# Optimization experiments

Hardware: AMD Instinct MI355X
Metric: run time of the kernel (lower is better)

The kernel has to match this reference:

```python
import jax, jax.numpy as jnp
import numpy as np

D_MODEL = 2048
NUM_HEADS = 16
HEAD_DIM = D_MODEL // NUM_HEADS
SCALE = 1.0 / np.sqrt(HEAD_DIM).astype(np.float32)
NEG_INF = -1e9


def setup_inputs() -> dict:
    key = jax.random.key(0)
    ks = jax.random.split(key, 10)
    B, S = 2, 2048
    x = jax.random.normal(ks[0], (B, S, D_MODEL), dtype=jnp.float32)
    # causal lower-triangular mask, broadcastable over (B, H)
    causal_mask = jnp.tril(jnp.ones((S, S), dtype=jnp.int32))[None, None]
    init = 1.0 / np.sqrt(D_MODEL)
    def lin(kw, kb):
        W = jax.random.uniform(kw, (D_MODEL, D_MODEL), jnp.float32, -init, init)
        b = jax.random.uniform(kb, (D_MODEL,), jnp.float32, -init, init)
        return W, b
    Wq, bq = lin(ks[1], ks[2])
    Wk, bk = lin(ks[3], ks[4])
    Wv, bv = lin(ks[5], ks[6])
    Wo, bo = lin(ks[7], ks[8])
    return {"x": x, "causal_mask": causal_mask,
            "Wq": Wq, "bq": bq, "Wk": Wk, "bk": bk,
            "Wv": Wv, "bv": bv, "Wo": Wo, "bo": bo}


def reference(x, causal_mask, Wq, bq, Wk, bk, Wv, bv, Wo, bo):
    B, S, _ = x.shape
    def proj(W, b):
        # torch Linear: x @ W.T + b -> (B, H, S, Dh)
        y = jnp.einsum('bsd,ed->bse', x, W) + b
        return y.reshape(B, S, NUM_HEADS, HEAD_DIM).transpose(0, 2, 1, 3)
    q = proj(Wq, bq)
    k = proj(Wk, bk)
    v = proj(Wv, bv)
    # apply_rope is a no-op stub in the source; q, k unchanged.
    scores = jnp.einsum('bhqd,bhkd->bhqk', q, k) * SCALE
    scores = jnp.where(causal_mask == 0, NEG_INF, scores)
    attn = jax.nn.softmax(scores, axis=-1)
    out = jnp.einsum('bhqk,bhkd->bhqd', attn, v)
    out = out.transpose(0, 2, 1, 3).reshape(B, S, D_MODEL)
    return jnp.einsum('bsd,ed->bse', out, Wo) + bo
```

## Files before the change

kernel.cpp:

```cpp
#include <hip/hip_runtime.h>
#include <hip/hip_bf16.h>
#include <stdint.h>
#include <stddef.h>

typedef __bf16 bf16_t;
typedef __bf16 bf16x4_t __attribute__((ext_vector_type(4)));
typedef __bf16 bf16x8_t __attribute__((ext_vector_type(8)));
typedef float f32x4 __attribute__((ext_vector_type(4)));

#define D_MODEL 2048
#define NHEADS 16
#define HDIM 128
#define SEQ 2048
#define BATCH 2
#define MTOT (BATCH * SEQ)
#define SCALE_F 0.08838834764831845f
#define LOG2E 1.4426950408889634f
#define QSCALE (SCALE_F * LOG2E)
#define KT 32
#define NEGI -3.0e38f
#define MINIT -1.0e30f

#define AS1 __attribute__((address_space(1)))
#define AS3 __attribute__((address_space(3)))

__device__ __forceinline__ void load_lds16(const bf16_t* g, bf16_t* l) {
  __builtin_amdgcn_global_load_lds((AS1 void*)(g), (AS3 void*)(l), 16, 0, 0);
}

__global__ void cast_kernel(const float* __restrict__ src, bf16_t* __restrict__ dst, int n4) {
  int i = blockIdx.x * blockDim.x + threadIdx.x;
  if (i < n4) {
    float4 v = ((const float4*)src)[i];
    bf16x4_t o;
    o.x = (bf16_t)v.x; o.y = (bf16_t)v.y; o.z = (bf16_t)v.z; o.w = (bf16_t)v.w;
    ((bf16x4_t*)dst)[i] = o;
  }
}

__global__ void cast4_kernel(const float* __restrict__ s0, const float* __restrict__ s1,
                             const float* __restrict__ s2, const float* __restrict__ s3,
                             bf16_t* __restrict__ dst, int n4) {
  int i = blockIdx.x * blockDim.x + threadIdx.x;
  int y = blockIdx.y;
  if (i < n4) {
    const float* src = (y == 0) ? s0 : (y == 1) ? s1 : (y == 2) ? s2 : s3;
    float4 v = ((const float4*)src)[i];
    bf16x4_t o;
    o.x = (bf16_t)v.x; o.y = (bf16_t)v.y; o.z = (bf16_t)v.z; o.w = (bf16_t)v.w;
    ((bf16x4_t*)(dst + (size_t)y * D_MODEL * D_MODEL / 4 * 4))[i] = o;
  }
}

__global__ __launch_bounds__(256) void gemm_fused(
    const bf16_t* __restrict__ A, const bf16_t* __restrict__ Bm, int mode,
    const float* __restrict__ bias0, const float* __restrict__ bias1,
    const float* __restrict__ bias2,
    bf16_t* __restrict__ Qo, bf16_t* __restrict__ Ko, bf16_t* __restrict__ Vto,
    float* __restrict__ Out) {
  const int K = 2048;
  __shared__ __align__(16) bf16_t lA[128 * 64];
  __shared__ __align__(16) bf16_t lB[128 * 64];
  const int m0 = blockIdx.x * 128;
  const int n0 = blockIdx.y * 128;
  const int t = threadIdx.x;
  const int w = t >> 6, lane = t & 63;
  const int wm = w & 1, wn = w >> 1;
  const int la = lane & 15, lb = lane >> 4;

  f32x4 acc[4][4];
  f32x4 zero = {0.f, 0.f, 0.f, 0.f};
#pragma unroll
  for (int i = 0; i < 4; i++)
#pragma unroll
    for (int j = 0; j < 4; j++) acc[i][j] = zero;

  const int row0 = t >> 3, cc = t & 7;
  const int ccs = cc ^ (row0 & 7);
  const bf16_t* gA = A + (size_t)(m0 + row0) * K + ccs * 8;
  const bf16_t* gB = Bm + (size_t)(n0 + row0) * K + ccs * 8;
  bf16_t* sA = lA + t * 8;
  bf16_t* sB = lB + t * 8;

  for (int k0 = 0; k0 < K; k0 += 64) {
    __syncthreads();
#pragma unroll
    for (int i = 0; i < 4; i++)
      load_lds16(gA + k0 + (size_t)(32 * i) * K, sA + 2048 * i);
#pragma unroll
    for (int i = 0; i < 4; i++)
      load_lds16(gB + k0 + (size_t)(32 * i) * K, sB + 2048 * i);
    __syncthreads();
#pragma unroll
    for (int ks = 0; ks < 2; ks++) {
      bf16x8_t af[4], bfr[4];
#pragma unroll
      for (int mt = 0; mt < 4; mt++) {
        int row = wm * 64 + mt * 16 + la;
        af[mt] = *(const bf16x8_t*)(lA + row * 64 + (((ks * 4 + lb) ^ (la & 7)) * 8));
      }
#pragma unroll
      for (int nt = 0; nt < 4; nt++) {
        int row = wn * 64 + nt * 16 + la;
        bfr[nt] = *(const bf16x8_t*)(lB + row * 64 + (((ks * 4 + lb) ^ (la & 7)) * 8));
      }
#pragma unroll
      for (int mt = 0; mt < 4; mt++)
#pragma unroll
        for (int nt = 0; nt < 4; nt++)
          acc[mt][nt] = __builtin_amdgcn_mfma_f32_16x16x32_bf16(af[mt], bfr[nt], acc[mt][nt], 0, 0, 0);
    }
  }

  if (mode == 0) {
#pragma unroll
    for (int mt = 0; mt < 4; mt++) {
#pragma unroll
      for (int nt = 0; nt < 4; nt++) {
        int m = m0 + wm * 64 + mt * 16 + lb * 4;
        int n = n0 + wn * 64 + nt * 16 + la;
        int b = m >> 11, s = m & 2047;
        int which = n >> 11, hd = n & 2047;
        int h = hd >> 7, d = hd & 127;
        float bv = (which == 0 ? bias0 : which == 1 ? bias1 : bias2)[hd];
        f32x4 v = acc[mt][nt];
        if (which == 2) {
          bf16_t* dst = Vto + ((size_t)(b * NHEADS + h) * HDIM + d) * SEQ + s;
          bf16x4_t pk;
          pk.x = (bf16_t)(v.x + bv); pk.y = (bf16_t)(v.y + bv);
          pk.z = (bf16_t)(v.z + bv); pk.w = (bf16_t)(v.w + bv);
          *(bf16x4_t*)dst = pk;
        } else {
          float sc = (which == 0) ? QSCALE : 1.0f;
          bf16_t* dst = (which == 0 ? Qo : Ko) + ((size_t)(b * NHEADS + h) * SEQ + s) * HDIM + d;
          dst[0]        = (bf16_t)((v.x + bv) * sc);
          dst[HDIM]     = (bf16_t)((v.y + bv) * sc);
          dst[2 * HDIM] = (bf16_t)((v.z + bv) * sc);
          dst[3 * HDIM] = (bf16_t)((v.w + bv) * sc);
        }
      }
    }
  } else {
#pragma unroll
    for (int mt = 0; mt < 4; mt++) {
#pragma unroll
      for (int nt = 0; nt < 4; nt++) {
        int m = m0 + wm * 64 + mt * 16 + lb * 4;
        int n = n0 + wn * 64 + nt * 16 + la;
        float bv = bias0[n];
        f32x4 v = acc[mt][nt];
        float* dst = Out + (size_t)m * D_MODEL + n;
        dst[0]           = v.x + bv;
        dst[D_MODEL]     = v.y + bv;
        dst[2 * D_MODEL] = v.z + bv;
        dst[3 * D_MODEL] = v.w + bv;
      }
    }
  }
}

__global__ __launch_bounds__(256, 3) void flash_attn(
    const bf16_t* __restrict__ Q, const bf16_t* __restrict__ Kg,
    const bf16_t* __restrict__ Vt, bf16_t* __restrict__ O,
    bf16_t* __restrict__ PO, float* __restrict__ ML) {
  __shared__ __align__(16) bf16_t lK[2][KT * 128];
  __shared__ __align__(16) bf16_t lV[2][128 * KT];
  __shared__ __align__(16) bf16_t lP[128 * 40];
  const int g = blockIdx.x;
  const int bh = g & 31, idx = g >> 5;
  const int t = threadIdx.x;
  const int w = t >> 6, lane = t & 63;
  const int la = lane & 15, lb = lane >> 4;
  const int qloc = w * 32 + la;

  const bf16_t* Qb = Q + (size_t)bh * SEQ * HDIM;
  const bf16_t* Kb = Kg + (size_t)bh * SEQ * HDIM;
  const bf16_t* Vb = Vt + (size_t)bh * HDIM * SEQ;
  const int b = bh >> 4, h = bh & 15;

  int nph, qts[2], k0s[2], k1s[2], slots[2];
  bool parts[2];
  if (idx < 8) {
    nph = 1; qts[0] = 8 + idx; k0s[0] = 0; k1s[0] = 34;
    parts[0] = true; slots[0] = (idx * 32 + bh) * 2;
  } else {
    int qtA = idx - 8;
    nph = 2;
    qts[0] = qtA; k0s[0] = 0; k1s[0] = 4 * qtA + 4; parts[0] = false; slots[0] = 0;
    qts[1] = 15 - qtA; k0s[1] = 34; k1s[1] = 64 - 4 * qtA;
    parts[1] = true; slots[1] = ((7 - qtA) * 32 + bh) * 2 + 1;
  }

  const int kj = t >> 4, kcc = t & 15;
  const int vd = t >> 2, vjc = t & 3;

  for (int ph = 0; ph < nph; ph++) {
    const int qt = qts[ph], kt0 = k0s[ph], kt1 = k1s[ph];
    const int q0 = qt * 128;

    bf16x8_t qf[2][4];
#pragma unroll
    for (int mt = 0; mt < 2; mt++)
#pragma unroll
      for (int ks = 0; ks < 4; ks++)
        qf[mt][ks] = *(const bf16x8_t*)(Qb + (size_t)(q0 + qloc + mt * 16) * HDIM + ks * 32 + lb * 8);

    f32x4 oacc[2][8];
    float mr[2] = {MINIT, MINIT}, lr[2] = {0.f, 0.f};
    f32x4 zero = {0.f, 0.f, 0.f, 0.f};
#pragma unroll
    for (int mt = 0; mt < 2; mt++)
#pragma unroll
      for (int dt = 0; dt < 8; dt++) oacc[mt][dt] = zero;

    __syncthreads();
    {
      const int j0 = kt0 * KT;
      int buf = kt0 & 1;
#pragma unroll
      for (int i = 0; i < 2; i++) {
        int j = kj + 16 * i;
        load_lds16(Kb + (size_t)(j0 + j) * HDIM + (((kcc ^ (j & 15))) * 8),
                   lK[buf] + (t + 256 * i) * 8);
      }
#pragma unroll
      for (int i = 0; i < 2; i++) {
        int d = vd + 64 * i;
        load_lds16(Vb + (size_t)d * SEQ + j0 + (((vjc ^ ((d & 3) ^ ((d >> 2) & 3)))) * 8),
                   lV[buf] + (t + 256 * i) * 8);
      }
    }

    for (int kt = kt0; kt < kt1; kt++) {
      const int j0 = kt * KT;
      const int cur = kt & 1;
      __syncthreads();

      if (kt + 1 < kt1) {
        const int jn = (kt + 1) * KT;
        const int nb = cur ^ 1;
#pragma unroll
        for (int i = 0; i < 2; i++) {
          int j = kj + 16 * i;
          load_lds16(Kb + (size_t)(jn + j) * HDIM + (((kcc ^ (j & 15))) * 8),
                     lK[nb] + (t + 256 * i) * 8);
        }
#pragma unroll
        for (int i = 0; i < 2; i++) {
          int d = vd + 64 * i;
          load_lds16(Vb + (size_t)d * SEQ + jn + (((vjc ^ ((d & 3) ^ ((d >> 2) & 3)))) * 8),
                     lV[nb] + (t + 256 * i) * 8);
        }
      }

      f32x4 st[2][2];
#pragma unroll
      for (int nt = 0; nt < 2; nt++)
#pragma unroll
        for (int mt = 0; mt < 2; mt++) st[nt][mt] = zero;
#pragma unroll
      for (int ks = 0; ks < 4; ks++) {
#pragma unroll
        for (int nt = 0; nt < 2; nt++) {
          int j = nt * 16 + la;
          int ck = (ks * 4 + lb) ^ (j & 15);
          bf16x8_t kf = *(const bf16x8_t*)(lK[cur] + j * 128 + ck * 8);
#pragma unroll
          for (int mt = 0; mt < 2; mt++)
            st[nt][mt] = __builtin_amdgcn_mfma_f32_16x16x32_bf16(kf, qf[mt][ks], st[nt][mt], 0, 0, 0);
        }
      }

      const bool dm = (j0 + KT > q0);
#pragma unroll
      for (int mt = 0; mt < 2; mt++) {
        int qg = q0 + qloc + mt * 16;
        if (dm) {
#pragma unroll
          for (int nt = 0; nt < 2; nt++)
#pragma unroll
            for (int r = 0; r < 4; r++)
              if (j0 + nt * 16 + lb * 4 + r > qg) st[nt][mt][r] = NEGI;
        }
        float tm = NEGI;
#pragma unroll
        for (int nt = 0; nt < 2; nt++)
#pragma unroll
          for (int r = 0; r < 4; r++) tm = fmaxf(tm, st[nt][mt][r]);
        tm = fmaxf(tm, __shfl_xor(tm, 16));
        tm = fmaxf(tm, __shfl_xor(tm, 32));
        float mnew = fmaxf(mr[mt], tm);
        float alpha = exp2f(mr[mt] - mnew);
        mr[mt] = mnew;
        lr[mt] *= alpha;
#pragma unroll
        for (int dt = 0; dt < 8; dt++) oacc[mt][dt] *= alpha;
        float s = 0.f;
#pragma unroll
        for (int nt = 0; nt < 2; nt++) {
          f32x4 p;
#pragma unroll
          for (int r = 0; r < 4; r++) {
            p[r] = exp2f(st[nt][mt][r] - mnew);
            s += p[r];
          }
          bf16x4_t pk;
          pk.x = (bf16_t)p[0]; pk.y = (bf16_t)p[1]; pk.z = (bf16_t)p[2]; pk.w = (bf16_t)p[3];
          *(bf16x4_t*)(lP + (qloc + mt * 16) * 40 + nt * 16 + lb * 4) = pk;
        }
        s += __shfl_xor(s, 16);
        s += __shfl_xor(s, 32);
        lr[mt] += s;
      }

      bf16x8_t pf[2];
#pragma unroll
      for (int mt = 0; mt < 2; mt++)
        pf[mt] = *(const bf16x8_t*)(lP + (w * 32 + mt * 16 + la) * 40 + lb * 8);
#pragma unroll
      for (int dt = 0; dt < 8; dt++) {
        int d = dt * 16 + la;
        int jc = lb ^ ((d & 3) ^ ((d >> 2) & 3));
        bf16x8_t vf = *(const bf16x8_t*)(lV[cur] + d * 32 + jc * 8);
#pragma unroll
        for (int mt = 0; mt < 2; mt++)
          oacc[mt][dt] = __builtin_amdgcn_mfma_f32_16x16x32_bf16(vf, pf[mt], oacc[mt][dt], 0, 0, 0);
      }
    }

    if (!parts[ph]) {
#pragma unroll
      for (int mt = 0; mt < 2; mt++) {
        float inv = 1.0f / lr[mt];
        int q = q0 + qloc + mt * 16;
        bf16_t* dst = O + ((size_t)b * SEQ + q) * D_MODEL + h * HDIM + lb * 4;
#pragma unroll
        for (int dt = 0; dt < 8; dt++) {
          f32x4 v = oacc[mt][dt];
          bf16x4_t pk;
          pk.x = (bf16_t)(v[0] * inv); pk.y = (bf16_t)(v[1] * inv);
          pk.z = (bf16_t)(v[2] * inv); pk.w = (bf16_t)(v[3] * inv);
          *(bf16x4_t*)(dst + dt * 16) = pk;
        }
      }
    } else {
      const int slot = slots[ph];
      bf16_t* pob = PO + (size_t)slot * 128 * 128;
#pragma unroll
      for (int mt = 0; mt < 2; mt++) {
        int q = qloc + mt * 16;
        bf16_t* dst = pob + (size_t)q * 128 + lb * 4;
#pragma unroll
        for (int dt = 0; dt < 8; dt++) {
          f32x4 v = oacc[mt][dt];
          bf16x4_t pk;
          pk.x = (bf16_t)v[0]; pk.y = (bf16_t)v[1];
          pk.z = (bf16_t)v[2]; pk.w = (bf16_t)v[3];
          *(bf16x4_t*)(dst + dt * 16) = pk;
        }
        if (lb == 0) {
          float2 ml = make_float2(mr[mt], lr[mt]);
          *(float2*)(ML + ((size_t)slot * 128 + q) * 2) = ml;
        }
      }
    }
  }
}

__global__ void merge_kernel(const bf16_t* __restrict__ PO, const float* __restrict__ ML,
                             bf16_t* __restrict__ O) {
  const int qti = blockIdx.x >> 5, bh = blockIdx.x & 31;
  const int qt = 8 + qti;
  const int t = threadIdx.x;
  const int q = t >> 1, dh = (t & 1) * 64;
  const size_t s1 = ((size_t)(qti * 32 + bh)) * 2;
  const float* ml1 = ML + (s1 * 128 + q) * 2;
  const float* ml2 = ML + ((s1 + 1) * 128 + q) * 2;
  float m1 = ml1[0], l1 = ml1[1], m2 = ml2[0], l2 = ml2[1];
  float m = fmaxf(m1, m2);
  float w1 = exp2f(m1 - m), w2 = exp2f(m2 - m);
  float inv = 1.0f / (w1 * l1 + w2 * l2);
  w1 *= inv; w2 *= inv;
  const bf16_t* p1 = PO + (s1 * 128 + q) * 128 + dh;
  const bf16_t* p2 = PO + ((s1 + 1) * 128 + q) * 128 + dh;
  const int b = bh >> 4, h = bh & 15;
  bf16_t* dst = O + ((size_t)b * SEQ + qt * 128 + q) * D_MODEL + h * HDIM + dh;
#pragma unroll
  for (int i = 0; i < 8; i++) {
    bf16x8_t a = ((const bf16x8_t*)p1)[i];
    bf16x8_t c = ((const bf16x8_t*)p2)[i];
    bf16x8_t o;
#pragma unroll
    for (int e = 0; e < 8; e++)
      o[e] = (bf16_t)(w1 * (float)a[e] + w2 * (float)c[e]);
    ((bf16x8_t*)dst)[i] = o;
  }
}

extern "C" void kernel_launch(void* const* d_in, const int* in_sizes, int n_in,
                              void* d_out, int out_size, void* d_ws, size_t ws_size,
                              hipStream_t stream) {
  (void)in_sizes; (void)n_in; (void)out_size; (void)ws_size;
  const float* x  = (const float*)d_in[0];
  const float* Wq = (const float*)d_in[2];
  const float* bq = (const float*)d_in[3];
  const float* Wk = (const float*)d_in[4];
  const float* bk = (const float*)d_in[5];
  const float* Wv = (const float*)d_in[6];
  const float* bv = (const float*)d_in[7];
  const float* Wo = (const float*)d_in[8];
  const float* bo = (const float*)d_in[9];
  float* out = (float*)d_out;

  const size_t NBF = (size_t)MTOT * D_MODEL * sizeof(bf16_t);
  const size_t WBF = (size_t)D_MODEL * D_MODEL * sizeof(bf16_t);
  char* p = (char*)d_ws;
  bf16_t* xb   = (bf16_t*)p; p += NBF;
  bf16_t* Wcat = (bf16_t*)p; p += 4 * WBF;
  bf16_t* Qb   = (bf16_t*)p; p += NBF;
  bf16_t* Kb   = (bf16_t*)p; p += NBF;
  bf16_t* Vtb  = (bf16_t*)p; p += NBF;
  bf16_t* Wob  = Wcat + (size_t)3 * D_MODEL * D_MODEL;
  bf16_t* Ob   = xb;
  bf16_t* PO = Wcat;
  float*  ML = (float*)(Wcat + (size_t)512 * 128 * 128);

  const int WN4 = D_MODEL * D_MODEL / 4;
  const int XN4 = MTOT * D_MODEL / 4;
  cast_kernel<<<XN4 / 256, 256, 0, stream>>>(x, xb, XN4);
  cast4_kernel<<<dim3(WN4 / 256, 4), 256, 0, stream>>>(Wq, Wk, Wv, Wo, Wcat, WN4);

  gemm_fused<<<dim3(MTOT / 128, 6144 / 128), 256, 0, stream>>>(
      xb, Wcat, 0, bq, bk, bv, Qb, Kb, Vtb, nullptr);

  flash_attn<<<dim3(512), 256, 0, stream>>>(Qb, Kb, Vtb, Ob, PO, ML);
  merge_kernel<<<dim3(256), 256, 0, stream>>>(PO, ML, Ob);

  gemm_fused<<<dim3(MTOT / 128, D_MODEL / 128), 256, 0, stream>>>(
      Ob, Wob, 1, bo, nullptr, nullptr, nullptr, nullptr, nullptr, out);
}
```

Before: 394.4 us.

## Use 256x256 double-buffered GEMM kernel for fused QKV projection

Adds a dedicated QKV projection kernel with 256x256 output tiles, 512 threads and double-buffered LDS staging, using direct global-to-LDS loads interleaved with MFMA phases and priority hints. Larger tiles raise arithmetic intensity and cut global traffic per FLOP, while the two-stage pipeline overlaps loads with compute. In exchange it uses 128KB of LDS per block and grows register pressure, and the grid drops to 384 blocks on 256 CUs, which may leave tail imbalance.

```diff
diff --git a/kernel.cpp b/kernel.cpp
--- a/kernel.cpp
+++ b/kernel.cpp
@@ -49,6 +49,159 @@
     bf16x4_t o;
     o.x = (bf16_t)v.x; o.y = (bf16_t)v.y; o.z = (bf16_t)v.z; o.w = (bf16_t)v.w;
     ((bf16x4_t*)(dst + (size_t)y * D_MODEL * D_MODEL / 4 * 4))[i] = o;
+  }
+}
+
+__global__ __launch_bounds__(512, 2) void gemm256_qkv(
+    const bf16_t* __restrict__ A, const bf16_t* __restrict__ Bm,
+    const float* __restrict__ bias0, const float* __restrict__ bias1,
+    const float* __restrict__ bias2,
+    bf16_t* __restrict__ Qo, bf16_t* __restrict__ Ko, bf16_t* __restrict__ Vto) {
+  const int K = 2048;
+  __shared__ __align__(16) bf16_t lA[2][256 * 64];
+  __shared__ __align__(16) bf16_t lB[2][256 * 64];
+  const int m0 = blockIdx.x * 256;
+  const int n0 = blockIdx.y * 256;
+  const int t = threadIdx.x;
+  const int w = t >> 6, lane = t & 63;
+  const int wm = w & 1, wn = w >> 1;
+  const int la = lane & 15, lb = lane >> 4;
+
+  f32x4 acc[8][4];
+  f32x4 zero = {0.f, 0.f, 0.f, 0.f};
+#pragma unroll
+  for (int i = 0; i < 8; i++)
+#pragma unroll
+    for (int j = 0; j < 4; j++) acc[i][j] = zero;
+
+  const int row0 = t >> 3, cc = t & 7;
+  const int ccs = cc ^ (row0 & 7);
+  const bf16_t* gA = A + (size_t)(m0 + row0) * K + ccs * 8;
+  const bf16_t* gB = Bm + (size_t)(n0 + row0) * K + ccs * 8;
+
+  auto stageA = [&](int buf, int k0) {
+#pragma unroll
+    for (int i = 0; i < 4; i++)
+      load_lds16(gA + k0 + (size_t)(64 * i) * K, &lA[buf][0] + (t + 512 * i) * 8);
+  };
+  auto stageB = [&](int buf, int k0) {
+#pragma unroll
+    for (int i = 0; i < 4; i++)
+      load_lds16(gB + k0 + (size_t)(64 * i) * K, &lB[buf][0] + (t + 512 * i) * 8);
+  };
+
+  bf16x8_t bfr[4][2];
+  bf16x8_t af[2][2];
+  auto loadBf = [&](int buf) {
+#pragma unroll
+    for (int nt = 0; nt < 4; nt++)
+#pragma unroll
+      for (int ks = 0; ks < 2; ks++) {
+        int row = wn * 64 + nt * 16 + la;
+        bfr[nt][ks] = *(const bf16x8_t*)(&lB[buf][0] + row * 64 + (((ks * 4 + lb) ^ (la & 7)) * 8));
+      }
+  };
+  auto loadAf = [&](int buf, int mt0) {
+#pragma unroll
+    for (int q = 0; q < 2; q++)
+#pragma unroll
+      for (int ks = 0; ks < 2; ks++) {
+        int row = wm * 128 + (mt0 + q) * 16 + la;
+        af[q][ks] = *(const bf16x8_t*)(&lA[buf][0] + row * 64 + (((ks * 4 + lb) ^ (la & 7)) * 8));
+      }
+  };
+  auto mfma16 = [&](int mt0) {
+#pragma unroll
+    for (int ks = 0; ks < 2; ks++)
+#pragma unroll
+      for (int q = 0; q < 2; q++)
+#pragma unroll
+        for (int nt = 0; nt < 4; nt++)
+          acc[mt0 + q][nt] =
+              __builtin_amdgcn_mfma_f32_16x16x32_bf16(af[q][ks], bfr[nt][ks], acc[mt0 + q][nt], 0, 0, 0);
+  };
+
+  stageA(0, 0); stageB(0, 0);
+  stageA(1, 64); stageB(1, 64);
+  asm volatile("s_waitcnt vmcnt(8)" ::: "memory");
+  __builtin_amdgcn_s_barrier();
+
+  for (int kt = 0; kt < 32; kt++) {
+    const int buf = kt & 1;
+    const int kn = (kt + 2) * 64;
+    const bool pre = (kt + 2 < 32);
+
+    loadBf(buf);
+    loadAf(buf, 0);
+    __builtin_amdgcn_s_barrier();
+    asm volatile("s_waitcnt lgkmcnt(0)" ::: "memory");
+    __builtin_amdgcn_sched_barrier(0);
+    __builtin_amdgcn_s_setprio(1);
+    mfma16(0);
+    __builtin_amdgcn_s_setprio(0);
+    __builtin_amdgcn_s_barrier();
+
+    loadAf(buf, 2);
+    if (pre) stageB(buf, kn);
+    __builtin_amdgcn_s_barrier();
+    asm volatile("s_waitcnt lgkmcnt(0)" ::: "memory");
+    __builtin_amdgcn_sched_barrier(0);
+    __builtin_amdgcn_s_setprio(1);
+    mfma16(2);
+    __builtin_amdgcn_s_setprio(0);
+    __builtin_amdgcn_s_barrier();
+
+    loadAf(buf, 4);
+    __builtin_amdgcn_s_barrier();
+    asm volatile("s_waitcnt lgkmcnt(0)" ::: "memory");
+    __builtin_amdgcn_sched_barrier(0);
+    __builtin_amdgcn_s_setprio(1);
+    mfma16(4);
+    __builtin_amdgcn_s_setprio(0);
+    __builtin_amdgcn_s_barrier();
+
+    loadAf(buf, 6);
+    __builtin_amdgcn_s_barrier();
+    if (pre) {
+      stageA(buf, kn);
+      asm volatile("s_waitcnt vmcnt(8)" ::: "memory");
+    } else {
+      asm volatile("s_waitcnt vmcnt(0)" ::: "memory");
+    }
+    asm volatile("s_waitcnt lgkmcnt(0)" ::: "memory");
+    __builtin_amdgcn_sched_barrier(0);
+    __builtin_amdgcn_s_setprio(1);
+    mfma16(6);
+    __builtin_amdgcn_s_setprio(0);
+    __builtin_amdgcn_s_barrier();
+  }
+
+#pragma unroll
+  for (int mt = 0; mt < 8; mt++) {
+#pragma unroll
+    for (int nt = 0; nt < 4; nt++) {
+      int m = m0 + wm * 128 + mt * 16 + lb * 4;
+      int n = n0 + wn * 64 + nt * 16 + la;
+      int bb = m >> 11, s = m & 2047;
+      int which = n >> 11, hd = n & 2047;
+      int h = hd >> 7, d = hd & 127;
+      float bv = (which == 0 ? bias0 : which == 1 ? bias1 : bias2)[hd];
+      f32x4 v = acc[mt][nt];
+      if (which == 2) {
+        bf16_t* dst = Vto + ((size_t)(bb * NHEADS + h) * HDIM + d) * SEQ + s;
+        bf16x4_t pk;
+        pk.x = (bf16_t)(v.x + bv); pk.y = (bf16_t)(v.y + bv);
+        pk.z = (bf16_t)(v.z + bv); pk.w = (bf16_t)(v.w + bv);
+        *(bf16x4_t*)dst = pk;
+      } else {
+        float sc = (which == 0) ? QSCALE : 1.0f;
+        bf16_t* dst = (which == 0 ? Qo : Ko) + ((size_t)(bb * NHEADS + h) * SEQ + s) * HDIM + d;
+        dst[0]        = (bf16_t)((v.x + bv) * sc);
+        dst[HDIM]     = (bf16_t)((v.y + bv) * sc);
+        dst[2 * HDIM] = (bf16_t)((v.z + bv) * sc);
+        dst[3 * HDIM] = (bf16_t)((v.w + bv) * sc);
+      }
+    }
   }
 }
 
@@ -430,8 +583,8 @@
   cast_kernel<<<XN4 / 256, 256, 0, stream>>>(x, xb, XN4);
   cast4_kernel<<<dim3(WN4 / 256, 4), 256, 0, stream>>>(Wq, Wk, Wv, Wo, Wcat, WN4);
 
-  gemm_fused<<<dim3(MTOT / 128, 6144 / 128), 256, 0, stream>>>(
-      xb, Wcat, 0, bq, bk, bv, Qb, Kb, Vtb, nullptr);
+  gemm256_qkv<<<dim3(MTOT / 256, 6144 / 256), 512, 0, stream>>>(
+      xb, Wcat, bq, bk, bv, Qb, Kb, Vtb);
 
   flash_attn<<<dim3(512), 256, 0, stream>>>(Qb, Kb, Vtb, Ob, PO, ML);
   merge_kernel<<<dim3(256), 256, 0, stream>>>(PO, ML, Ob);
```

After: 412.3 us. +4.5%, slower.

## Double key tile size, single-buffer V with in-iteration load, defer softmax rescale

Applied to the files above, without the earlier changes.

The flash-attention key tile grows from 32 to 64 columns, so each block runs half as many loop iterations. V is now single-buffered and loaded at the start of the same iteration, overlapping with the QK^T matmul and softmax, with an explicit vmcnt wait and barrier before PV. K stays double-buffered. The online-softmax rescale is skipped unless the new row max exceeds the running max by more than a threshold, which trims exp and multiply work. The larger LDS footprint lowers the occupancy target from 3 to 2 blocks, and lazy rescaling can let unnormalised P values grow up to 2^8.

```diff
diff --git a/kernel.cpp b/kernel.cpp
--- a/kernel.cpp
+++ b/kernel.cpp
@@ -17,9 +17,10 @@
 #define SCALE_F 0.08838834764831845f
 #define LOG2E 1.4426950408889634f
 #define QSCALE (SCALE_F * LOG2E)
-#define KT 32
+#define KT 64
 #define NEGI -3.0e38f
 #define MINIT -1.0e30f
+#define DEFER_THR 8.0f
 
 #define AS1 __attribute__((address_space(1)))
 #define AS3 __attribute__((address_space(3)))
@@ -159,13 +160,13 @@
   }
 }
 
-__global__ __launch_bounds__(256, 3) void flash_attn(
+__global__ __launch_bounds__(256, 2) void flash_attn(
     const bf16_t* __restrict__ Q, const bf16_t* __restrict__ Kg,
     const bf16_t* __restrict__ Vt, bf16_t* __restrict__ O,
     bf16_t* __restrict__ PO, float* __restrict__ ML) {
   __shared__ __align__(16) bf16_t lK[2][KT * 128];
-  __shared__ __align__(16) bf16_t lV[2][128 * KT];
-  __shared__ __align__(16) bf16_t lP[128 * 40];
+  __shared__ __align__(16) bf16_t lV[128 * KT];
+  __shared__ __align__(16) bf16_t lP[128 * 72];
   const int g = blockIdx.x;
   const int bh = g & 31, idx = g >> 5;
   const int t = threadIdx.x;
@@ -181,18 +182,20 @@
   int nph, qts[2], k0s[2], k1s[2], slots[2];
   bool parts[2];
   if (idx < 8) {
-    nph = 1; qts[0] = 8 + idx; k0s[0] = 0; k1s[0] = 34;
+    nph = 1; qts[0] = 8 + idx; k0s[0] = 0; k1s[0] = 17;
     parts[0] = true; slots[0] = (idx * 32 + bh) * 2;
   } else {
     int qtA = idx - 8;
     nph = 2;
-    qts[0] = qtA; k0s[0] = 0; k1s[0] = 4 * qtA + 4; parts[0] = false; slots[0] = 0;
-    qts[1] = 15 - qtA; k0s[1] = 34; k1s[1] = 64 - 4 * qtA;
+    qts[0] = qtA; k0s[0] = 0; k1s[0] = 2 * qtA + 2; parts[0] = false; slots[0] = 0;
+    qts[1] = 15 - qtA; k0s[1] = 17; k1s[1] = 32 - 2 * qtA;
     parts[1] = true; slots[1] = ((7 - qtA) * 32 + bh) * 2 + 1;
   }
 
-  const int kj = t >> 4, kcc = t & 15;
-  const int vd = t >> 2, vjc = t & 3;
+  const int krow = t >> 4, kcc = t & 15;
+  const int kccx = kcc ^ krow;
+  const int vrow = t >> 3, vjc = t & 7;
+  const int vccx = vjc ^ (vrow & 7);
 
   for (int ph = 0; ph < nph; ph++) {
     const int qt = qts[ph], kt0 = k0s[ph], kt1 = k1s[ph];
@@ -213,57 +216,44 @@
 #pragma unroll
       for (int dt = 0; dt < 8; dt++) oacc[mt][dt] = zero;
 
-    __syncthreads();
     {
       const int j0 = kt0 * KT;
-      int buf = kt0 & 1;
-#pragma unroll
-      for (int i = 0; i < 2; i++) {
-        int j = kj + 16 * i;
-        load_lds16(Kb + (size_t)(j0 + j) * HDIM + (((kcc ^ (j & 15))) * 8),
-                   lK[buf] + (t + 256 * i) * 8);
-      }
-#pragma unroll
-      for (int i = 0; i < 2; i++) {
-        int d = vd + 64 * i;
-        load_lds16(Vb + (size_t)d * SEQ + j0 + (((vjc ^ ((d & 3) ^ ((d >> 2) & 3)))) * 8),
-                   lV[buf] + (t + 256 * i) * 8);
-      }
+#pragma unroll
+      for (int i = 0; i < 4; i++)
+        load_lds16(Kb + (size_t)(j0 + krow + 16 * i) * HDIM + kccx * 8,
+                   lK[kt0 & 1] + (t + 256 * i) * 8);
     }
 
     for (int kt = kt0; kt < kt1; kt++) {
       const int j0 = kt * KT;
       const int cur = kt & 1;
+      const bool pre = (kt + 1 < kt1);
+
       __syncthreads();
 
-      if (kt + 1 < kt1) {
+#pragma unroll
+      for (int i = 0; i < 4; i++)
+        load_lds16(Vb + (size_t)(vrow + 32 * i) * SEQ + j0 + vccx * 8,
+                   lV + (t + 256 * i) * 8);
+      if (pre) {
         const int jn = (kt + 1) * KT;
-        const int nb = cur ^ 1;
-#pragma unroll
-        for (int i = 0; i < 2; i++) {
-          int j = kj + 16 * i;
-          load_lds16(Kb + (size_t)(jn + j) * HDIM + (((kcc ^ (j & 15))) * 8),
-                     lK[nb] + (t + 256 * i) * 8);
-        }
-#pragma unroll
-        for (int i = 0; i < 2; i++) {
-          int d = vd + 64 * i;
-          load_lds16(Vb + (size_t)d * SEQ + jn + (((vjc ^ ((d & 3) ^ ((d >> 2) & 3)))) * 8),
-                     lV[nb] + (t + 256 * i) * 8);
-        }
-      }
-
-      f32x4 st[2][2];
-#pragma unroll
-      for (int nt = 0; nt < 2; nt++)
+#pragma unroll
+        for (int i = 0; i < 4; i++)
+          load_lds16(Kb + (size_t)(jn + krow + 16 * i) * HDIM + kccx * 8,
+                     lK[cur ^ 1] + (t + 256 * i) * 8);
+      }
+
+      f32x4 st[4][2];
+#pragma unroll
+      for (int nt = 0; nt < 4; nt++)
 #pragma unroll
         for (int mt = 0; mt < 2; mt++) st[nt][mt] = zero;
 #pragma unroll
       for (int ks = 0; ks < 4; ks++) {
 #pragma unroll
-        for (int nt = 0; nt < 2; nt++) {
+        for (int nt = 0; nt < 4; nt++) {
           int j = nt * 16 + la;
-          int ck = (ks * 4 + lb) ^ (j & 15);
+          int ck = (ks * 4 + lb) ^ la;
           bf16x8_t kf = *(const bf16x8_t*)(lK[cur] + j * 128 + ck * 8);
 #pragma unroll
           for (int mt = 0; mt < 2; mt++)
@@ -277,54 +267,68 @@
         int qg = q0 + qloc + mt * 16;
         if (dm) {
 #pragma unroll
-          for (int nt = 0; nt < 2; nt++)
+          for (int nt = 0; nt < 4; nt++)
 #pragma unroll
             for (int r = 0; r < 4; r++)
               if (j0 + nt * 16 + lb * 4 + r > qg) st[nt][mt][r] = NEGI;
         }
         float tm = NEGI;
 #pragma unroll
-        for (int nt = 0; nt < 2; nt++)
+        for (int nt = 0; nt < 4; nt++)
 #pragma unroll
           for (int r = 0; r < 4; r++) tm = fmaxf(tm, st[nt][mt][r]);
         tm = fmaxf(tm, __shfl_xor(tm, 16));
         tm = fmaxf(tm, __shfl_xor(tm, 32));
-        float mnew = fmaxf(mr[mt], tm);
-        float alpha = exp2f(mr[mt] - mnew);
-        mr[mt] = mnew;
-        lr[mt] *= alpha;
-#pragma unroll
-        for (int dt = 0; dt < 8; dt++) oacc[mt][dt] *= alpha;
+        if (!__all(tm - mr[mt] <= DEFER_THR)) {
+          float mnew = fmaxf(mr[mt], tm);
+          float alpha = exp2f(mr[mt] - mnew);
+          lr[mt] *= alpha;
+#pragma unroll
+          for (int dt = 0; dt < 8; dt++) oacc[mt][dt] *= alpha;
+          mr[mt] = mnew;
+        }
         float s = 0.f;
 #pragma unroll
-        for (int nt = 0; nt < 2; nt++) {
+        for (int nt = 0; nt < 4; nt++) {
           f32x4 p;
 #pragma unroll
           for (int r = 0; r < 4; r++) {
-            p[r] = exp2f(st[nt][mt][r] - mnew);
+            p[r] = exp2f(st[nt][mt][r] - mr[mt]);
             s += p[r];
           }
           bf16x4_t pk;
           pk.x = (bf16_t)p[0]; pk.y = (bf16_t)p[1]; pk.z = (bf16_t)p[2]; pk.w = (bf16_t)p[3];
-          *(bf16x4_t*)(lP + (qloc + mt * 16) * 40 + nt * 16 + lb * 4) = pk;
+          *(bf16x4_t*)(lP + (qloc + mt * 16) * 72 + nt * 16 + lb * 4) = pk;
         }
         s += __shfl_xor(s, 16);
         s += __shfl_xor(s, 32);
         lr[mt] += s;
       }
 
-      bf16x8_t pf[2];
+      if (pre) {
+        asm volatile("s_waitcnt vmcnt(4)" ::: "memory");
+      } else {
+        asm volatile("s_waitcnt vmcnt(0)" ::: "memory");
+      }
+      __builtin_amdgcn_s_barrier();
+
+      bf16x8_t pf[2][2];
 #pragma unroll
       for (int mt = 0; mt < 2; mt++)
-        pf[mt] = *(const bf16x8_t*)(lP + (w * 32 + mt * 16 + la) * 40 + lb * 8);
+#pragma unroll
+        for (int ksv = 0; ksv < 2; ksv++)
+          pf[mt][ksv] = *(const bf16x8_t*)(lP + (w * 32 + mt * 16 + la) * 72 + ksv * 32 + lb * 8);
 #pragma unroll
       for (int dt = 0; dt < 8; dt++) {
         int d = dt * 16 + la;
-        int jc = lb ^ ((d & 3) ^ ((d >> 2) & 3));
-        bf16x8_t vf = *(const bf16x8_t*)(lV[cur] + d * 32 + jc * 8);
-#pragma unroll
-        for (int mt = 0; mt < 2; mt++)
-          oacc[mt][dt] = __builtin_amdgcn_mfma_f32_16x16x32_bf16(vf, pf[mt], oacc[mt][dt], 0, 0, 0);
+#pragma unroll
+        for (int ksv = 0; ksv < 2; ksv++) {
+          int jc = (ksv * 4 + lb) ^ (d & 7);
+          bf16x8_t vf = *(const bf16x8_t*)(lV + d * 64 + jc * 8);
+#pragma unroll
+          for (int mt = 0; mt < 2; mt++)
+            oacc[mt][dt] = __builtin_amdgcn_mfma_f32_16x16x32_bf16(vf, pf[mt][ksv], oacc[mt][dt], 0, 0, 0);
+        }
       }
     }
 
```

New measurement: 375.2 us. 1.05x faster.
